# Kernel tuning notes

Hardware: AMD Instinct MI355X
Metric: run time of the kernel (lower is better)

Reference implementation:

```python
import jax, jax.numpy as jnp
import numpy as np

THRESHOLD = 0.5
N_SEG = 5
NEG_INF = -1e30
EPS = 1e-12  # F.normalize eps


def setup_inputs() -> dict:
    key = jax.random.key(0)
    kx, kl = jax.random.split(key)
    B, D, L = 4096, 512, 80
    x = jax.random.normal(kx, (B, D), dtype=jnp.float32)
    labels = jax.random.randint(kl, (B, L), 0, 2, dtype=jnp.int32)
    return {"x": x, "labels": labels}


def reference(x, labels):
    B = x.shape[0]
    labels_f = labels.astype(jnp.float32)
    # pairwise Jaccard over multi-hot labels
    intersection = labels_f @ labels_f.T                      # [B, B]
    counts = labels_f.sum(axis=1, keepdims=True)              # [B, 1]
    union = counts + counts.T - intersection
    jaccard = intersection / union                            # [B, B]
    # cosine similarity (F.normalize with eps clamp)
    norm = jnp.maximum(jnp.linalg.norm(x, axis=1, keepdims=True), EPS)
    nx = x / norm
    sim = nx @ nx.T                                           # [B, B]
    # --- sample positive (uniform among jaccard > threshold), fixed key ---
    pos_mask = jaccard > THRESHOLD
    valid_mask = jnp.any(pos_mask, axis=1)                    # [B]
    logits = jnp.where(pos_mask, 0.0, NEG_INF)
    sampled = jax.random.categorical(jax.random.key(42), logits, axis=-1)
    pos_samples = jnp.where(valid_mask, sampled, 0)           # invalid rows -> 0
    # --- top-k negatives: jaccard strictly below the positive's jaccard ---
    pos_sim_j = jaccard[jnp.arange(B), pos_samples]           # [B]
    neg_mask = jaccard < pos_sim_j[:, None]
    neg_sims = jnp.where(neg_mask, jaccard, -jnp.inf)
    _, neg_samples = jax.lax.top_k(neg_sims, N_SEG)           # [B, N_SEG]
    # --- contrastive loss on cosine sims at sampled indices ---
    rel_pos = sim[jnp.arange(B), pos_samples]                 # [B]
    rel_neg = jnp.take_along_axis(sim, neg_samples, axis=1)   # [B, N_SEG]
    exp_pos = jnp.exp(rel_pos)
    sum_exp_neg = jnp.exp(rel_neg).sum(axis=1)
    loss = -jnp.log(exp_pos / (exp_pos + sum_exp_neg))
    vm = valid_mask.astype(x.dtype)
    return (loss * vm).sum() / vm.sum()
```

## Files before the change

kernel.cpp:

```cpp
#include <hip/hip_runtime.h>
#include <stdint.h>

#define B_ROWS 4096
#define DIMS   512
#define NLAB   80
#define HALF_ROWS 2048
#define HCNT   8388608u
#define CHUNK  1024
#define SEGCAP 512u
#define NBLK   2048

typedef unsigned long long u64;

__device__ __forceinline__ uint32_t rotl32(uint32_t x, uint32_t d) {
    return (x << d) | (x >> (32u - d));
}

__device__ __forceinline__ void tf2x32_key42(uint32_t c0, uint32_t c1,
                                             uint32_t& o0, uint32_t& o1) {
    const uint32_t ks0 = 0u;
    const uint32_t ks1 = 42u;
    const uint32_t ks2 = 0x1BD11BDAu ^ 0u ^ 42u;
    uint32_t x0 = c0 + ks0;
    uint32_t x1 = c1 + ks1;
#define TF_RND(r) { x0 += x1; x1 = rotl32(x1, (r)); x1 ^= x0; }
    TF_RND(13u) TF_RND(15u) TF_RND(26u) TF_RND(6u)
    x0 += ks1; x1 += ks2 + 1u;
    TF_RND(17u) TF_RND(29u) TF_RND(16u) TF_RND(24u)
    x0 += ks2; x1 += ks0 + 2u;
    TF_RND(13u) TF_RND(15u) TF_RND(26u) TF_RND(6u)
    x0 += ks0; x1 += ks1 + 3u;
    TF_RND(17u) TF_RND(29u) TF_RND(16u) TF_RND(24u)
    x0 += ks1; x1 += ks2 + 4u;
    TF_RND(13u) TF_RND(15u) TF_RND(26u) TF_RND(6u)
    x0 += ks2; x1 += ks0 + 5u;
#undef TF_RND
    o0 = x0; o1 = x1;
}

__device__ __forceinline__ u64 shflx64(u64 v, int m) {
    uint32_t lo = __shfl_xor((uint32_t)(v & 0xFFFFFFFFull), m, 64);
    uint32_t hi = __shfl_xor((uint32_t)(v >> 32), m, 64);
    return ((u64)hi << 32) | (u64)lo;
}

__device__ __forceinline__ uint32_t umx(uint32_t a, uint32_t b) { return a > b ? a : b; }
__device__ __forceinline__ uint32_t umn(uint32_t a, uint32_t b) { return a < b ? a : b; }

__device__ __forceinline__ uint32_t mbcnt64(u64 m) {
    uint32_t c = __builtin_amdgcn_mbcnt_lo((uint32_t)m, 0u);
    return __builtin_amdgcn_mbcnt_hi((uint32_t)(m >> 32), c);
}

__device__ __forceinline__ void ins5_u32(uint32_t* t, uint32_t k) {
    t[4] = umx(t[4], k);
    uint32_t hi, lo;
    hi = umx(t[3], t[4]); lo = umn(t[3], t[4]); t[3] = hi; t[4] = lo;
    hi = umx(t[2], t[3]); lo = umn(t[2], t[3]); t[2] = hi; t[3] = lo;
    hi = umx(t[1], t[2]); lo = umn(t[1], t[2]); t[1] = hi; t[2] = lo;
    hi = umx(t[0], t[1]); lo = umn(t[0], t[1]); t[0] = hi; t[1] = lo;
}

__device__ __forceinline__ void merge5_u32(uint32_t* A, const uint32_t* Bv) {
    uint32_t a0=A[0],a1=A[1],a2=A[2],a3=A[3],a4=A[4];
    uint32_t b0=Bv[0],b1=Bv[1],b2=Bv[2],b3=Bv[3],b4=Bv[4];
    uint32_t m0 = umx(a0, b0);
    uint32_t m1 = umx(umx(a1, b1), umn(a0, b0));
    uint32_t m2 = umx(umx(a2, b2), umx(umn(a0, b1), umn(a1, b0)));
    uint32_t m3 = umx(umx(a3, b3), umx(umx(umn(a0, b2), umn(a1, b1)), umn(a2, b0)));
    uint32_t m4 = umx(umx(a4, b4), umx(umx(umn(a0, b3), umn(a1, b2)),
                                       umx(umn(a2, b1), umn(a3, b0))));
    A[0]=m0; A[1]=m1; A[2]=m2; A[3]=m3; A[4]=m4;
}

__device__ __forceinline__ void wave_top5_2(uint32_t* ta, uint32_t* tb,
                                            uint32_t* fa, uint32_t* fb) {
#pragma unroll
    for (int k = 0; k < 5; ++k) {
        uint32_t ma = ta[0], mb = tb[0];
#pragma unroll
        for (int s = 1; s < 64; s <<= 1) {
            ma = umx(ma, __shfl_xor(ma, s, 64));
            mb = umx(mb, __shfl_xor(mb, s, 64));
        }
        fa[k] = ma; fb[k] = mb;
        if (ta[0] == ma) { ta[0]=ta[1]; ta[1]=ta[2]; ta[2]=ta[3]; ta[3]=ta[4]; ta[4]=0u; }
        if (tb[0] == mb) { tb[0]=tb[1]; tb[1]=tb[2]; tb[2]=tb[3]; tb[3]=tb[4]; tb[4]=0u; }
    }
}

__device__ __forceinline__ uint32_t jkey19(uint32_t it, uint32_t u) {
    const uint32_t n = it << 19;
    float f = (float)it * __builtin_amdgcn_rcpf((float)u) * 524288.0f;
    uint32_t ak = (uint32_t)f;
    int r = (int)(n - ak * u);
    if (r < 0) { ak--; r += (int)u; }
    if (r >= (int)u) ak++;
    return ak + 1u;
}


__global__ __launch_bounds__(256) void prep_kernel(const float* __restrict__ x,
                                                   const int* __restrict__ labels,
                                                   uint4* __restrict__ pk,
                                                   float* __restrict__ norms) {
    const int tid = threadIdx.x;
    const int lane = tid & 63;
    const int row = blockIdx.x * 4 + (tid >> 6);
    const int* lr = labels + (size_t)row * NLAB;
    const int la = lr[lane];
    const int lb = (lane < 16) ? lr[64 + lane] : 0;
    const u64 b0 = __ballot(la != 0);
    const u64 b1 = __ballot(lb != 0);
    const uint32_t w2 = (uint32_t)b1 & 0xFFFFu;
    const uint32_t cnt = (uint32_t)__popcll(b0) + (uint32_t)__popc(w2);
    if (lane == 0) pk[row] = make_uint4((uint32_t)b0, (uint32_t)(b0 >> 32), w2, cnt);
    const float* xr = x + (size_t)row * DIMS;
    float ss = 0.f;
#pragma unroll
    for (int u = 0; u < 8; ++u) { float v = xr[lane + 64 * u]; ss += v * v; }
#pragma unroll
    for (int m = 1; m < 64; m <<= 1) ss += __shfl_xor(ss, m, 64);
    if (lane == 0) norms[row] = fmaxf(sqrtf(ss), 1e-12f);
}

__global__ __launch_bounds__(256) void fused_kernel(const float* __restrict__ x,
                                                    const uint4* __restrict__ pk,
                                                    const float* __restrict__ norms,
                                                    float2* __restrict__ blockPart) {
    __shared__ uint32_t segL[2][4][SEGCAP];
    __shared__ uint32_t cntL[2][4];
    __shared__ u64      gpart[2][4];
    __shared__ uint32_t keysL[2][4][5];
    __shared__ uint32_t posL[2], pjkeyL[2], validL[2];
    __shared__ uint32_t tgL[2][6];
    __shared__ float    simsL[2][6];
    __shared__ float    lossW[2], cntW2[2];

    const int tid = threadIdx.x;
    const int lane = tid & 63;
    const int sub  = tid >> 6;
    const int pr   = (int)blockIdx.x;
    const int r0 = pr, r1 = pr + HALF_ROWS;
    const uint4 P0 = pk[r0], P1 = pk[r1];
    const uint32_t cw0 = P0.w, cw1 = P1.w;
    const int jbase = sub * CHUNK;

    uint32_t cnt0 = 0u, cnt1 = 0u;
#pragma unroll 8
    for (int jb = 0; jb < CHUNK; jb += 64) {
        const int j = jbase + jb + lane;
        const uint4 pj = pk[j];
        const uint32_t cj = pj.w;
        const uint32_t it0 = (uint32_t)(__popc(P0.x & pj.x) + __popc(P0.y & pj.y) + __popc(P0.z & pj.z));
        const uint32_t u0  = cw0 + cj - it0;
        const uint32_t it1 = (uint32_t)(__popc(P1.x & pj.x) + __popc(P1.y & pj.y) + __popc(P1.z & pj.z));
        const uint32_t u1  = cw1 + cj - it1;
        const bool b0 = __umul24(it0, 20u) >= __umul24(u0, 9u);
        const bool b1 = __umul24(it1, 20u) >= __umul24(u1, 9u);
        const u64 bal0 = __ballot(b0);
        const u64 bal1 = __ballot(b1);
        if (b0) {
            const uint32_t off = cnt0 + mbcnt64(bal0);
            if (off < SEGCAP) segL[0][sub][off] = (it0 << 20) | (u0 << 12) | (uint32_t)j;
        }
        cnt0 += (uint32_t)__popcll(bal0);
        if (b1) {
            const uint32_t off = cnt1 + mbcnt64(bal1);
            if (off < SEGCAP) segL[1][sub][off] = (it1 << 20) | (u1 << 12) | (uint32_t)j;
        }
        cnt1 += (uint32_t)__popcll(bal1);
    }
    if (lane == 0) { cntL[0][sub] = cnt0; cntL[1][sub] = cnt1; }
    __syncthreads();

    const uint32_t base23 = (uint32_t)pr * (uint32_t)B_ROWS;
#pragma unroll
    for (int h = 0; h < 2; ++h) {
        const int n = (int)umn(cntL[h][sub], SEGCAP);
        u64 gb = 0ull;
        for (int e = lane; e < n; e += 64) {
            const uint32_t ent = segL[h][sub][e];
            const uint32_t u  = (ent >> 12) & 0xFFu;
            const uint32_t it = ent >> 20;
            if ((it << 1) > u) {
                const uint32_t j = ent & 0xFFFu;
                uint32_t o0, o1;
                tf2x32_key42(base23 + j, base23 + j + HCNT, o0, o1);
                const uint32_t o = h ? o1 : o0;
                const u64 key = ((u64)(o >> 9) << 41) | ((u64)((~j) & 0xFFFu) << 29) | (u64)jkey19(it, u);
                if (key > gb) gb = key;
            }
        }
#pragma unroll
        for (int m = 1; m < 64; m <<= 1) {
            const u64 o = shflx64(gb, m);
            if (o > gb) gb = o;
        }
        if (lane == 0) gpart[h][sub] = gb;
    }
    __syncthreads();

    if (sub < 2 && lane == 0) {
        const int h = sub;
        u64 g = gpart[h][0];
        if (gpart[h][1] > g) g = gpart[h][1];
        if (gpart[h][2] > g) g = gpart[h][2];
        if (gpart[h][3] > g) g = gpart[h][3];
        const bool valid = g != 0ull;
        validL[h] = valid ? 1u : 0u;
        posL[h]   = valid ? ((~(uint32_t)(g >> 29)) & 0xFFFu) : 0u;
        pjkeyL[h] = (uint32_t)(g & 0xFFFFFu);
    }
    __syncthreads();

    {
        const uint32_t pj0 = pjkeyL[0], pj1 = pjkeyL[1];
        const int n0 = (int)umn(cntL[0][sub], SEGCAP);
        const int n1 = (int)umn(cntL[1][sub], SEGCAP);
        uint32_t t0[5] = {0u,0u,0u,0u,0u}, t1[5] = {0u,0u,0u,0u,0u};
        for (int e = lane; e < n0; e += 64) {
            const uint32_t ent = segL[0][sub][e];
            const uint32_t j  = ent & 0xFFFu;
            const uint32_t u  = (ent >> 12) & 0xFFu;
            const uint32_t it = ent >> 20;
            const uint32_t k19 = jkey19(it, u);
            const uint32_t key = (k19 < pj0) ? ((k19 << 12) | ((~j) & 0xFFFu)) : 0u;
            ins5_u32(t0, key);
        }
        for (int e = lane; e < n1; e += 64) {
            const uint32_t ent = segL[1][sub][e];
            const uint32_t j  = ent & 0xFFFu;
            const uint32_t u  = (ent >> 12) & 0xFFu;
            const uint32_t it = ent >> 20;
            const uint32_t k19 = jkey19(it, u);
            const uint32_t key = (k19 < pj1) ? ((k19 << 12) | ((~j) & 0xFFFu)) : 0u;
            ins5_u32(t1, key);
        }
        uint32_t f0[5], f1[5];
        wave_top5_2(t0, t1, f0, f1);
        if (lane == 0) {
#pragma unroll
            for (int k = 0; k < 5; ++k) { keysL[0][sub][k] = f0[k]; keysL[1][sub][k] = f1[k]; }
        }
    }
    __syncthreads();

    if (sub < 2 && lane == 0) {
        const int h = sub;
        uint32_t f[5];
#pragma unroll
        for (int k = 0; k < 5; ++k) f[k] = keysL[h][0][k];
#pragma unroll
        for (int s = 1; s < 4; ++s) merge5_u32(f, keysL[h][s]);
        tgL[h][0] = posL[h];
#pragma unroll
        for (int k = 0; k < 5; ++k) tgL[h][k + 1] = (~f[k]) & 0xFFFu;
    }
    __syncthreads();

#pragma unroll
    for (int k = 0; k < 3; ++k) {
        const int d = sub + 4 * k;
        const int h = (d >= 6) ? 1 : 0;
        const int q = d - 6 * h;
        const int row = h ? r1 : r0;
        const int tgt = (int)tgL[h][q];
        const float* pa = x + (size_t)row * DIMS;
        const float* pb = x + (size_t)tgt * DIMS;
        float s = 0.f;
#pragma unroll
        for (int u = 0; u < 8; ++u) s += pa[lane + 64 * u] * pb[lane + 64 * u];
#pragma unroll
        for (int m = 1; m < 64; m <<= 1) s += __shfl_xor(s, m, 64);
        if (lane == 0) simsL[h][q] = s;
    }
    __syncthreads();

    if (sub < 2 && lane == 0) {
        const int h = sub;
        float loss = 0.f, cnt = 0.f;
        if (validL[h]) {
            const int row = h ? r1 : r0;
            const float nr = norms[row];
            const float sp = simsL[h][0] / (nr * norms[tgL[h][0]]);
            float sen = 0.f;
#pragma unroll
            for (int q = 1; q < 6; ++q) sen += expf(simsL[h][q] / (nr * norms[tgL[h][q]]));
            const float ep = expf(sp);
            loss = -logf(ep / (ep + sen));
            cnt = 1.f;
        }
        lossW[h] = loss; cntW2[h] = cnt;
    }
    __syncthreads();
    if (tid == 0) blockPart[pr] = make_float2(lossW[0] + lossW[1], cntW2[0] + cntW2[1]);
}

__global__ __launch_bounds__(256) void final_kernel(const float2* __restrict__ blockPart,
                                                    float* __restrict__ out) {
    __shared__ float rl[4], rc[4];
    const int tid = threadIdx.x;
    const int lane = tid & 63;
    const int w = tid >> 6;
    float sl = 0.f, sc = 0.f;
#pragma unroll
    for (int k = 0; k < 8; ++k) {
        const float2 p = blockPart[tid + 256 * k];
        sl += p.x; sc += p.y;
    }
#pragma unroll
    for (int m = 1; m < 64; m <<= 1) {
        sl += __shfl_xor(sl, m, 64);
        sc += __shfl_xor(sc, m, 64);
    }
    if (lane == 0) { rl[w] = sl; rc[w] = sc; }
    __syncthreads();
    if (tid == 0) out[0] = (rl[0] + rl[1] + rl[2] + rl[3]) / (rc[0] + rc[1] + rc[2] + rc[3]);
}

extern "C" void kernel_launch(void* const* d_in, const int* in_sizes, int n_in,
                              void* d_out, int out_size, void* d_ws, size_t ws_size,
                              hipStream_t stream) {
    const float* x      = (const float*)d_in[0];
    const int*   labels = (const int*)d_in[1];
    float* out = (float*)d_out;

    char* ws = (char*)d_ws;
    uint4*  pk    = (uint4*)ws;
    float*  norms = (float*)(ws + 65536);
    float2* bPart = (float2*)(ws + 65536 + 16384);

    hipLaunchKernelGGL(prep_kernel,  dim3(1024), dim3(256), 0, stream, x, labels, pk, norms);
    hipLaunchKernelGGL(fused_kernel, dim3(NBLK), dim3(256), 0, stream, x, pk, norms, bPart);
    hipLaunchKernelGGL(final_kernel, dim3(1),    dim3(256), 0, stream, bPart, out);
}
```

Before: 87.40 us.

## Split fused scan/select kernel into separate selection, dot-product, and loss kernels

The fused kernel is split into three parts. A scan/select kernel writes the positive and negative target indices plus validity flags to a workspace. A separate dots kernel computes the 12 per-block dot products, one wave per task, and the final kernel now evaluates the losses itself. The aim is to drop x from the scan kernel, which should lower its register and LDS pressure and remove its tail syncs, so the dot products can run at full occupancy. In exchange it adds an extra launch, global round trips for indices and sims, and a heavier single-block final reduction.

```diff
diff --git a/kernel.cpp b/kernel.cpp
--- a/kernel.cpp
+++ b/kernel.cpp
@@ -9,6 +9,7 @@
 #define CHUNK  1024
 #define SEGCAP 512u
 #define NBLK   2048
+#define NTASK  (NBLK * 12)
 
 typedef unsigned long long u64;
 
@@ -124,18 +125,13 @@
     if (lane == 0) norms[row] = fmaxf(sqrtf(ss), 1e-12f);
 }
 
-__global__ __launch_bounds__(256) void fused_kernel(const float* __restrict__ x,
-                                                    const uint4* __restrict__ pk,
-                                                    const float* __restrict__ norms,
-                                                    float2* __restrict__ blockPart) {
+__global__ __launch_bounds__(256) void scan_sel_kernel(const uint4* __restrict__ pk,
+                                                       uint32_t* __restrict__ tgv) {
     __shared__ uint32_t segL[2][4][SEGCAP];
     __shared__ uint32_t cntL[2][4];
     __shared__ u64      gpart[2][4];
     __shared__ uint32_t keysL[2][4][5];
     __shared__ uint32_t posL[2], pjkeyL[2], validL[2];
-    __shared__ uint32_t tgL[2][6];
-    __shared__ float    simsL[2][6];
-    __shared__ float    lossW[2], cntW2[2];
 
     const int tid = threadIdx.x;
     const int lane = tid & 63;
@@ -253,51 +249,39 @@
         for (int k = 0; k < 5; ++k) f[k] = keysL[h][0][k];
 #pragma unroll
         for (int s = 1; s < 4; ++s) merge5_u32(f, keysL[h][s]);
-        tgL[h][0] = posL[h];
-#pragma unroll
-        for (int k = 0; k < 5; ++k) tgL[h][k + 1] = (~f[k]) & 0xFFFu;
-    }
-    __syncthreads();
-
-#pragma unroll
-    for (int k = 0; k < 3; ++k) {
-        const int d = sub + 4 * k;
-        const int h = (d >= 6) ? 1 : 0;
-        const int q = d - 6 * h;
-        const int row = h ? r1 : r0;
-        const int tgt = (int)tgL[h][q];
-        const float* pa = x + (size_t)row * DIMS;
-        const float* pb = x + (size_t)tgt * DIMS;
-        float s = 0.f;
-#pragma unroll
-        for (int u = 0; u < 8; ++u) s += pa[lane + 64 * u] * pb[lane + 64 * u];
-#pragma unroll
-        for (int m = 1; m < 64; m <<= 1) s += __shfl_xor(s, m, 64);
-        if (lane == 0) simsL[h][q] = s;
-    }
-    __syncthreads();
-
-    if (sub < 2 && lane == 0) {
-        const int h = sub;
-        float loss = 0.f, cnt = 0.f;
-        if (validL[h]) {
-            const int row = h ? r1 : r0;
-            const float nr = norms[row];
-            const float sp = simsL[h][0] / (nr * norms[tgL[h][0]]);
-            float sen = 0.f;
-#pragma unroll
-            for (int q = 1; q < 6; ++q) sen += expf(simsL[h][q] / (nr * norms[tgL[h][q]]));
-            const float ep = expf(sp);
-            loss = -logf(ep / (ep + sen));
-            cnt = 1.f;
-        }
-        lossW[h] = loss; cntW2[h] = cnt;
-    }
-    __syncthreads();
-    if (tid == 0) blockPart[pr] = make_float2(lossW[0] + lossW[1], cntW2[0] + cntW2[1]);
-}
-
-__global__ __launch_bounds__(256) void final_kernel(const float2* __restrict__ blockPart,
+        uint32_t* o = tgv + (size_t)pr * 16;
+        o[h * 6 + 0] = posL[h];
+#pragma unroll
+        for (int k = 0; k < 5; ++k) o[h * 6 + k + 1] = (~f[k]) & 0xFFFu;
+        o[12 + h] = validL[h];
+    }
+}
+
+__global__ __launch_bounds__(256) void dots_kernel(const float* __restrict__ x,
+                                                   const uint32_t* __restrict__ tgv,
+                                                   float* __restrict__ sims) {
+    const int tid = threadIdx.x;
+    const int lane = tid & 63;
+    const int w = tid >> 6;
+    const int task = (int)blockIdx.x * 4 + w;
+    const int pr = task / 12;
+    const int d  = task - pr * 12;
+    const int h  = (d >= 6) ? 1 : 0;
+    const int row = h ? pr + HALF_ROWS : pr;
+    const int tgt = (int)tgv[(size_t)pr * 16 + d];
+    const float* pa = x + (size_t)row * DIMS;
+    const float* pb = x + (size_t)tgt * DIMS;
+    float s = 0.f;
+#pragma unroll
+    for (int u = 0; u < 8; ++u) s += pa[lane + 64 * u] * pb[lane + 64 * u];
+#pragma unroll
+    for (int m = 1; m < 64; m <<= 1) s += __shfl_xor(s, m, 64);
+    if (lane == 0) sims[(size_t)pr * 12 + d] = s;
+}
+
+__global__ __launch_bounds__(256) void final_kernel(const uint32_t* __restrict__ tgv,
+                                                    const float* __restrict__ sims,
+                                                    const float* __restrict__ norms,
                                                     float* __restrict__ out) {
     __shared__ float rl[4], rc[4];
     const int tid = threadIdx.x;
@@ -306,8 +290,26 @@
     float sl = 0.f, sc = 0.f;
 #pragma unroll
     for (int k = 0; k < 8; ++k) {
-        const float2 p = blockPart[tid + 256 * k];
-        sl += p.x; sc += p.y;
+        const int pr = tid + 256 * k;
+        const uint32_t* tg = tgv + (size_t)pr * 16;
+        const float* sm = sims + (size_t)pr * 12;
+        float pl = 0.f, pc = 0.f;
+#pragma unroll
+        for (int h = 0; h < 2; ++h) {
+            if (tg[12 + h]) {
+                const int row = h ? pr + HALF_ROWS : pr;
+                const float nr = norms[row];
+                const float sp = sm[h * 6] / (nr * norms[tg[h * 6]]);
+                float sen = 0.f;
+#pragma unroll
+                for (int q = 1; q < 6; ++q)
+                    sen += expf(sm[h * 6 + q] / (nr * norms[tg[h * 6 + q]]));
+                const float ep = expf(sp);
+                pl += -logf(ep / (ep + sen));
+                pc += 1.f;
+            }
+        }
+        sl += pl; sc += pc;
     }
 #pragma unroll
     for (int m = 1; m < 64; m <<= 1) {
@@ -327,11 +329,13 @@
     float* out = (float*)d_out;
 
     char* ws = (char*)d_ws;
-    uint4*  pk    = (uint4*)ws;
-    float*  norms = (float*)(ws + 65536);
-    float2* bPart = (float2*)(ws + 65536 + 16384);
-
-    hipLaunchKernelGGL(prep_kernel,  dim3(1024), dim3(256), 0, stream, x, labels, pk, norms);
-    hipLaunchKernelGGL(fused_kernel, dim3(NBLK), dim3(256), 0, stream, x, pk, norms, bPart);
-    hipLaunchKernelGGL(final_kernel, dim3(1),    dim3(256), 0, stream, bPart, out);
-}
+    uint4*    pk    = (uint4*)ws;
+    float*    norms = (float*)(ws + 65536);
+    uint32_t* tgv   = (uint32_t*)(ws + 81920);
+    float*    sims  = (float*)(ws + 81920 + 131072);
+
+    hipLaunchKernelGGL(prep_kernel,     dim3(1024), dim3(256), 0, stream, x, labels, pk, norms);
+    hipLaunchKernelGGL(scan_sel_kernel, dim3(NBLK), dim3(256), 0, stream, pk, tgv);
+    hipLaunchKernelGGL(dots_kernel,     dim3(NTASK / 4), dim3(256), 0, stream, x, tgv, sims);
+    hipLaunchKernelGGL(final_kernel,    dim3(1),    dim3(256), 0, stream, tgv, sims, norms, out);
+}
```

Measured after the change: 108.2 us. +23.8%, slower.
